# Performance work log

Measured on AMD Instinct MI355X. Metric: run time of the kernel, lower is better.

The kernel has to match this reference:

```python
import jax, jax.numpy as jnp
import numpy as np

N = 8192        # nodes in batch
E = 262144      # edges (avg degree 32)
IN_C = 64
OUT_C = 64
K = 3           # max_k
G = 64          # graphs in batch
NC = 10         # n_class
EPS = 1e-5      # batchnorm eps


def setup_inputs() -> dict:
    key = jax.random.key(0)
    ks = jax.random.split(key, 16)
    D_in = IN_C * K    # 192
    D_out = OUT_C * K  # 192
    inp = {
        'x': jax.random.normal(ks[0], (N, IN_C), jnp.float32),
        'edge_index': jax.random.randint(ks[1], (2, E), 0, N, dtype=jnp.int64),
        'batch': jnp.sort(jax.random.randint(ks[2], (N,), 0, G, dtype=jnp.int64)),
        # spectral-normed masked linear
        'W_orig': jax.random.normal(ks[3], (D_out, D_in), jnp.float32) * 0.05,
        'b': jnp.zeros((D_out,), jnp.float32),
        'u': jax.random.normal(ks[4], (D_out,), jnp.float32),
        # batchnorms (training-mode batch stats)
        'bn1_gamma': jnp.ones((D_out,), jnp.float32),
        'bn1_beta': jnp.zeros((D_out,), jnp.float32),
        'bn2_gamma': jnp.ones((D_out * 3,), jnp.float32),
        'bn2_beta': jnp.zeros((D_out * 3,), jnp.float32),
        # funnel head
        'w1': jax.random.normal(ks[5], (D_out * 2, D_out * 3), jnp.float32) * 0.05,
        'b1': jnp.zeros((D_out * 2,), jnp.float32),
        'w2': jax.random.normal(ks[6], (D_out, D_out * 2), jnp.float32) * 0.05,
        'b2': jnp.zeros((D_out,), jnp.float32),
        'w3': jax.random.normal(ks[7], (NC, D_out), jnp.float32) * 0.05,
        'b3': jnp.zeros((NC,), jnp.float32),
    }
    return inp


def _forward(x, edge_index, batch, W_orig, b, u, bn1_gamma, bn1_beta,
             bn2_gamma, bn2_beta, w1, b1, w2, b2, w3, b3):
    n = x.shape[0]
    row, col = edge_index[0], edge_index[1]
    # sym-normalized Laplacian L = I - D^-1/2 A D^-1/2, densified ([N,N])
    deg = jnp.zeros((n,), x.dtype).at[row].add(1.0)
    dinv = jnp.where(deg > 0, jax.lax.rsqrt(jnp.maximum(deg, 1.0)), 0.0)
    vals = -dinv[row] * dinv[col]
    L = jnp.zeros((n, n), x.dtype).at[row, col].add(vals)
    idx = jnp.arange(n)
    L = L.at[idx, idx].add(1.0)
    Hs = [x]
    h = x
    for _ in range(K - 1):
        h = L @ h
        Hs.append(h)
    Hcat = jnp.concatenate(Hs, axis=1)              # [N, IN_C*K]
    # spectral norm of W (one power-iteration step with stored u)
    v = W_orig.T @ u
    v = v / (jnp.linalg.norm(v) + 1e-12)
    sigma = u @ (W_orig @ v)
    W = W_orig / sigma
    # block lower-triangular mask: block i passes first IN_C*(i+1) input cols
    col_idx = jnp.arange(IN_C * K)
    row_block = jnp.arange(OUT_C * K) // OUT_C
    mask = (col_idx[None, :] < IN_C * (row_block[:, None] + 1)).astype(W.dtype)
    H = Hcat @ (W * mask).T + b                     # masked linear
    # reservoir_act_fun is identity (default)
    mu, var = H.mean(0), H.var(0)                   # BN (batch stats)
    H = bn1_gamma * (H - mu) * jax.lax.rsqrt(var + EPS) + bn1_beta
    # fused-style triple pooling over graph ids
    Hsum = jax.ops.segment_sum(H, batch, num_segments=G)
    cnt = jax.ops.segment_sum(jnp.ones((n,), H.dtype), batch, num_segments=G)
    Havg = Hsum / jnp.maximum(cnt, 1.0)[:, None]
    Hmax = jax.ops.segment_max(H, batch, num_segments=G)
    Hg = jnp.concatenate([Havg, Hsum, Hmax], axis=1)  # [G, 3*OUT_C*K]
    mu2, var2 = Hg.mean(0), Hg.var(0)
    xo = bn2_gamma * (Hg - mu2) * jax.lax.rsqrt(var2 + EPS) + bn2_beta
    # funnel output (dropout = identity in eval)
    xo = jax.nn.relu(xo @ w1.T + b1)
    xo = jax.nn.relu(xo @ w2.T + b2)
    return jax.nn.log_softmax(xo @ w3.T + b3, axis=1)


def reference(x, edge_index, batch, W_orig, b, u, bn1_gamma, bn1_beta,
              bn2_gamma, bn2_beta, w1, b1, w2, b2, w3, b3):
    return _forward(x, edge_index, batch, W_orig, b, u, bn1_gamma, bn1_beta,
                    bn2_gamma, bn2_beta, w1, b1, w2, b2, w3, b3)
```

## Files before the change

kernel.cpp:

```cpp
#include <hip/hip_runtime.h>
#include <math.h>

#define NN   8192
#define EE   262144
#define CIN  64
#define DD   192
#define GG   64
#define NCLS 10
#define D3   576
#define F1   384
#define F2   192
#define EPSB 1e-5f
#define NB   64
#define EPB  (EE / NB)
#define PS   8

__global__ __launch_bounds__(1024) void prep_kernel(const float* __restrict__ W,
    const float* __restrict__ u, const float* __restrict__ w1,
    const float* __restrict__ w2, const int* __restrict__ batch,
    const int* __restrict__ ei,
    float* __restrict__ sig, int* __restrict__ gstart, int* __restrict__ pcnt,
    float* __restrict__ Wp, float* __restrict__ Wp1, float* __restrict__ Wp2) {
    __shared__ int hist[NN];
    int b = blockIdx.x, t = threadIdx.x;
    if (b < 324) {
        int idx = b * 1024 + t;
        if (idx < DD * DD) {
            int r = idx / DD, c = idx - r * DD;
            float m = (c < CIN * ((r >> 6) + 1)) ? 1.f : 0.f;
            Wp[((c >> 2) * DD + r) * 4 + (c & 3)] = m * W[idx];
        } else if (idx < DD * DD + F1 * D3) {
            int i1 = idx - DD * DD;
            int tt = i1 / D3, k = i1 - tt * D3;
            Wp1[((k >> 2) * F1 + tt) * 4 + (k & 3)] = w1[i1];
        } else {
            int i2 = idx - DD * DD - F1 * D3;
            int tt = i2 / F1, k = i2 - tt * F1;
            Wp2[((k >> 2) * F2 + tt) * 4 + (k & 3)] = w2[i2];
        }
        return;
    }
    if (b == 325) {
        for (int i = t; i < NN; i += 1024) {
            int b0 = batch[i];
            int b1 = (i + 1 < NN) ? batch[i + 1] : GG;
            if (i == 0) { for (int g = 0; g <= b0; g++) gstart[g] = 0; }
            for (int g = b0 + 1; g <= b1; g++) gstart[g] = i + 1;
        }
        return;
    }
    if (b >= 326) {
        int cb = b - 326;
        int4* hz = (int4*)hist;
        for (int i = t; i < NN / 4; i += 1024) hz[i] = make_int4(0, 0, 0, 0);
        __syncthreads();
        int e0 = cb * EPB;
        for (int i = t; i < EPB; i += 1024) atomicAdd(&hist[ei[e0 + i]], 1);
        __syncthreads();
        const int4* hs = (const int4*)hist;
        int4* p4 = (int4*)&pcnt[cb * NN];
        for (int i = t; i < NN / 4; i += 1024) p4[i] = hs[i];
        return;
    }
    float* vp  = (float*)hist;
    float* vsh = vp + 768;
    float* red = vsh + DD;
    if (t < 768) {
        int c = t >> 2, j = t & 3;
        float s = 0.f;
        const float* Wc = W + c;
        for (int i = j * 48; i < j * 48 + 48; i++) s += Wc[i * DD] * u[i];
        vp[t] = s;
    }
    __syncthreads();
    float vv = 0.f;
    if (t < DD) {
        float v = vp[4 * t] + vp[4 * t + 1] + vp[4 * t + 2] + vp[4 * t + 3];
        vsh[t] = v;
        vv = v * v;
    }
    red[t] = vv;
    __syncthreads();
    for (int off = 512; off > 0; off >>= 1) {
        if (t < off) red[t] += red[t + off];
        __syncthreads();
    }
    float norm = sqrtf(red[0]) + 1e-12f;
    __syncthreads();
    float a = 0.f;
    for (int idx = t; idx < DD * DD; idx += 1024) {
        int r = idx / DD, c = idx - r * DD;
        a += u[r] * W[idx] * vsh[c];
    }
    red[t] = a;
    __syncthreads();
    for (int off = 512; off > 0; off >>= 1) {
        if (t < off) red[t] += red[t + off];
        __syncthreads();
    }
    if (t == 0) sig[0] = norm / red[0];
}

__global__ __launch_bounds__(256) void offs_kernel(int* __restrict__ pcnt,
                                                   int* __restrict__ deg,
                                                   float* __restrict__ dinv) {
    int i = blockIdx.x * 256 + threadIdx.x;
    int run = 0;
#pragma unroll
    for (int b = 0; b < NB; b++) {
        int v = pcnt[b * NN + i];
        pcnt[b * NN + i] = run;
        run += v;
    }
    deg[i] = run;
    dinv[i] = (run > 0) ? rsqrtf((float)run) : 0.f;
}

__global__ __launch_bounds__(1024) void scatter_kernel(const int* __restrict__ ei,
                                                       const int* __restrict__ deg,
                                                       const int* __restrict__ off,
                                                       int* __restrict__ rowptr,
                                                       unsigned short* __restrict__ csr_col) {
    __shared__ int cur[NN];
    __shared__ int temp[1024];
    int b = blockIdx.x, t = threadIdx.x;
    int base = t * 8;
    int d[8], l[8];
    {
        const int4 a4 = *(const int4*)&deg[base];
        const int4 b4 = *(const int4*)&deg[base + 4];
        d[0] = a4.x; d[1] = a4.y; d[2] = a4.z; d[3] = a4.w;
        d[4] = b4.x; d[5] = b4.y; d[6] = b4.z; d[7] = b4.w;
    }
    int run = 0;
#pragma unroll
    for (int j = 0; j < 8; j++) { l[j] = run; run += d[j]; }
    temp[t] = run;
    __syncthreads();
    for (int o = 1; o < 1024; o <<= 1) {
        int v = (t >= o) ? temp[t - o] : 0;
        __syncthreads();
        temp[t] += v;
        __syncthreads();
    }
    int prefix = (t > 0) ? temp[t - 1] : 0;
    const int* ob = &off[b * NN];
#pragma unroll
    for (int j = 0; j < 8; j++) cur[base + j] = prefix + l[j] + ob[base + j];
    if (b == 0) {
#pragma unroll
        for (int j = 0; j < 8; j++) rowptr[base + j] = prefix + l[j];
        if (t == 1023) rowptr[NN] = temp[1023];
    }
    __syncthreads();
    int e0 = b * EPB;
    for (int i = t; i < EPB; i += 1024) {
        int r = ei[e0 + i];
        int c = ei[EE + e0 + i];
        int pos = atomicAdd(&cur[r], 1);
        csr_col[pos] = (unsigned short)c;
    }
}

__global__ __launch_bounds__(256) void spmm_kernel(const float* __restrict__ hin,
    int in_stride, int in_off,
    const int* __restrict__ rowptr, const unsigned short* __restrict__ col,
    const float* __restrict__ dinv,
    float* __restrict__ Hcat, int coff, int write_self) {
    int idx = blockIdx.x * 256 + threadIdx.x;
    int row = idx >> 6;
    int lane = idx & 63;
    int s = rowptr[row], e = rowptr[row + 1];
    float acc0 = 0.f, acc1 = 0.f;
    int p = s;
    for (; p + 1 < e; p += 2) {
        int c0 = col[p], c1 = col[p + 1];
        acc0 += dinv[c0] * hin[c0 * in_stride + in_off + lane];
        acc1 += dinv[c1] * hin[c1 * in_stride + in_off + lane];
    }
    if (p < e) {
        int c = col[p];
        acc0 += dinv[c] * hin[c * in_stride + in_off + lane];
    }
    float acc = acc0 + acc1;
    float self = hin[row * in_stride + in_off + lane];
    Hcat[row * DD + coff + lane] = self - dinv[row] * acc;
    if (write_self) Hcat[row * DD + lane] = self;
}

__global__ __launch_bounds__(192) void gemm_kernel(float* __restrict__ Hcat,
    const float* __restrict__ Wp, const float* __restrict__ bias,
    const float* __restrict__ sig) {
    __shared__ float hs[16 * DD];
    int t = threadIdx.x;
    int n0 = blockIdx.x * 16;
    const float4* src = (const float4*)&Hcat[n0 * DD];
    float4* dst = (float4*)hs;
#pragma unroll
    for (int i = 0; i < 4; i++) dst[t + 192 * i] = src[t + 192 * i];
    __syncthreads();
    float acc[16];
#pragma unroll
    for (int r = 0; r < 16; r++) acc[r] = 0.f;
    const float4* Wp4 = (const float4*)Wp;
    for (int k4 = 0; k4 < DD / 4; k4++) {
        float4 w = Wp4[k4 * DD + t];
#pragma unroll
        for (int r = 0; r < 16; r++) {
            const float4 h = *(const float4*)&hs[r * DD + k4 * 4];
            acc[r] += h.x * w.x + h.y * w.y + h.z * w.z + h.w * w.w;
        }
    }
    float inv_sigma = sig[0];
    float bv = bias[t];
#pragma unroll
    for (int r = 0; r < 16; r++) Hcat[(n0 + r) * DD + t] = inv_sigma * acc[r] + bv;
}

__global__ __launch_bounds__(192) void pool_kernel(const float* __restrict__ H,
    const int* __restrict__ gstart,
    float* __restrict__ Psum, float* __restrict__ Psq,
    float* __restrict__ Pmin, float* __restrict__ Pmax) {
    int b = blockIdx.x;
    int g = b >> 3, s = b & 7, c = threadIdx.x;
    int beg = gstart[g], end = gstart[g + 1];
    float sum = 0.f, sq = 0.f, mn = INFINITY, mx = -INFINITY;
    for (int i = beg + s; i < end; i += PS) {
        float x = H[i * DD + c];
        sum += x; sq += x * x;
        mn = fminf(mn, x); mx = fmaxf(mx, x);
    }
    Psum[b * DD + c] = sum; Psq[b * DD + c] = sq;
    Pmin[b * DD + c] = mn;  Pmax[b * DD + c] = mx;
}

__global__ __launch_bounds__(64) void hg_kernel(
    const float* __restrict__ Psum, const float* __restrict__ Psq,
    const float* __restrict__ Pmin, const float* __restrict__ Pmax,
    const int* __restrict__ gstart,
    const float* __restrict__ g1, const float* __restrict__ be1,
    const float* __restrict__ g2, const float* __restrict__ be2,
    float* __restrict__ Hg) {
    int t = blockIdx.x;
    int g = threadIdx.x;
    int f = t / DD, c = t - f * DD;
    float Sg = 0.f, Qg = 0.f;
#pragma unroll
    for (int s = 0; s < PS; s++) {
        Sg += Psum[(g * PS + s) * DD + c];
        Qg += Psq[(g * PS + s) * DD + c];
    }
    float S = Sg, Q = Qg;
    for (int off = 32; off > 0; off >>= 1) {
        S += __shfl_xor(S, off);
        Q += __shfl_xor(Q, off);
    }
    float mu = S * (1.f / (float)NN);
    float var = Q * (1.f / (float)NN) - mu * mu;
    float sc = g1[c] * rsqrtf(var + EPSB);
    float bb = be1[c];
    float v;
    if (f == 2) {
        float mx = -INFINITY, mn = INFINITY;
#pragma unroll
        for (int s = 0; s < PS; s++) {
            mx = fmaxf(mx, Pmax[(g * PS + s) * DD + c]);
            mn = fminf(mn, Pmin[(g * PS + s) * DD + c]);
        }
        float raw = (sc >= 0.f) ? mx : mn;
        v = sc * (raw - mu) + bb;
    } else {
        float nf = (float)(gstart[g + 1] - gstart[g]);
        float hsum = sc * (Sg - nf * mu) + nf * bb;
        v = (f == 0) ? hsum / fmaxf(nf, 1.f) : hsum;
    }
    float s2 = v, ss2 = v * v;
    for (int off = 32; off > 0; off >>= 1) {
        s2 += __shfl_xor(s2, off);
        ss2 += __shfl_xor(ss2, off);
    }
    float m2 = s2 * (1.f / (float)GG);
    float var2 = ss2 * (1.f / (float)GG) - m2 * m2;
    float sc2 = g2[t] * rsqrtf(var2 + EPSB);
    Hg[g * D3 + t] = sc2 * (v - m2) + be2[t];
}

__global__ __launch_bounds__(F1) void funnel_kernel(const float* __restrict__ Hg,
    const float* __restrict__ Wp1, const float* __restrict__ b1,
    const float* __restrict__ Wp2, const float* __restrict__ b2,
    const float* __restrict__ w3, const float* __restrict__ b3,
    float* __restrict__ out) {
    __shared__ float hg[D3];
    __shared__ float x1[F1];
    __shared__ float x2[F2];
    __shared__ float lg[NCLS];
    __shared__ float s_lse;
    int g = blockIdx.x, t = threadIdx.x;
    for (int i = t; i < D3; i += F1) hg[i] = Hg[g * D3 + i];
    __syncthreads();
    {
        float a = b1[t];
        const float4* W4 = (const float4*)Wp1;
        for (int k4 = 0; k4 < D3 / 4; k4++) {
            float4 w = W4[k4 * F1 + t];
            const float4 h = *(const float4*)&hg[k4 * 4];
            a += w.x * h.x + w.y * h.y + w.z * h.z + w.w * h.w;
        }
        x1[t] = fmaxf(a, 0.f);
    }
    __syncthreads();
    if (t < F2) {
        float a = b2[t];
        const float4* W4 = (const float4*)Wp2;
        for (int k4 = 0; k4 < F1 / 4; k4++) {
            float4 w = W4[k4 * F2 + t];
            const float4 h = *(const float4*)&x1[k4 * 4];
            a += w.x * h.x + w.y * h.y + w.z * h.z + w.w * h.w;
        }
        x2[t] = fmaxf(a, 0.f);
    }
    __syncthreads();
    if (t < NCLS) {
        float a = b3[t];
        const float4* wr = (const float4*)&w3[t * F2];
        const float4* h4 = (const float4*)x2;
        for (int k = 0; k < F2 / 4; k++) {
            float4 w = wr[k], h = h4[k];
            a += w.x * h.x + w.y * h.y + w.z * h.z + w.w * h.w;
        }
        lg[t] = a;
    }
    __syncthreads();
    if (t == 0) {
        float m = lg[0];
        for (int i = 1; i < NCLS; i++) m = fmaxf(m, lg[i]);
        float se = 0.f;
        for (int i = 0; i < NCLS; i++) se += expf(lg[i] - m);
        s_lse = m + logf(se);
    }
    __syncthreads();
    if (t < NCLS) out[g * NCLS + t] = lg[t] - s_lse;
}


extern "C" void kernel_launch(void* const* d_in, const int* in_sizes, int n_in,
                              void* d_out, int out_size, void* d_ws, size_t ws_size,
                              hipStream_t stream) {
    (void)in_sizes; (void)n_in; (void)out_size; (void)ws_size;
    const float* x     = (const float*)d_in[0];
    const int*   ei    = (const int*)d_in[1];
    const int*   batch = (const int*)d_in[2];
    const float* W     = (const float*)d_in[3];
    const float* b     = (const float*)d_in[4];
    const float* u     = (const float*)d_in[5];
    const float* g1    = (const float*)d_in[6];
    const float* be1   = (const float*)d_in[7];
    const float* g2    = (const float*)d_in[8];
    const float* be2   = (const float*)d_in[9];
    const float* w1    = (const float*)d_in[10];
    const float* b1    = (const float*)d_in[11];
    const float* w2    = (const float*)d_in[12];
    const float* b2    = (const float*)d_in[13];
    const float* w3    = (const float*)d_in[14];
    const float* b3    = (const float*)d_in[15];
    float* out = (float*)d_out;
    char*  ws  = (char*)d_ws;

    int*            gstart  = (int*)(ws + 0);
    int*            rowptr  = (int*)(ws + 512);
    int*            deg     = (int*)(ws + 33536);
    float*          dinv    = (float*)(ws + 66304);
    float*          sig     = (float*)(ws + 99072);
    float*          Wp      = (float*)(ws + 99328);
    float*          Psum    = (float*)(ws + 246784);
    float*          Psq     = (float*)(ws + 640000);
    float*          Pmin    = (float*)(ws + 1033216);
    float*          Pmax    = (float*)(ws + 1426432);
    float*          Hg      = (float*)(ws + 1819648);
    unsigned short* csr_col = (unsigned short*)(ws + 1967104);
    float*          Wp1     = (float*)(ws + 2491392);
    float*          Wp2     = (float*)(ws + 3376128);
    int*            pcnt    = (int*)(ws + 3671040);
    float*          Hcat    = (float*)(ws + 5768192);

    prep_kernel<<<326 + NB, 1024, 0, stream>>>(W, u, w1, w2, batch, ei,
                                               sig, gstart, pcnt, Wp, Wp1, Wp2);
    offs_kernel<<<NN / 256, 256, 0, stream>>>(pcnt, deg, dinv);
    scatter_kernel<<<NB, 1024, 0, stream>>>(ei, deg, pcnt, rowptr, csr_col);
    spmm_kernel<<<NN * 64 / 256, 256, 0, stream>>>(x, CIN, 0, rowptr, csr_col, dinv, Hcat, CIN, 1);
    spmm_kernel<<<NN * 64 / 256, 256, 0, stream>>>(Hcat, DD, CIN, rowptr, csr_col, dinv, Hcat, 2 * CIN, 0);
    gemm_kernel<<<NN / 16, 192, 0, stream>>>(Hcat, Wp, b, sig);
    pool_kernel<<<GG * PS, 192, 0, stream>>>(Hcat, gstart, Psum, Psq, Pmin, Pmax);
    hg_kernel<<<D3, 64, 0, stream>>>(Psum, Psq, Pmin, Pmax, gstart, g1, be1, g2, be2, Hg);
    funnel_kernel<<<GG, F1, 0, stream>>>(Hg, Wp1, b1, Wp2, b2, w3, b3, out);
}
```

Baseline: 200.3 us.

## Fuse masked GEMM with graph pooling via atomics; shrink partial counts to u16

The GEMM and pooling kernels are merged. Each GEMM block reduces its rows per graph and updates global per-graph sum, sum-of-squares, and max/min through atomics, using order-preserving uint keys for float max/min. The final H is no longer written back to Hcat, and the separate pooling pass is gone. Per-block edge histograms are stored as uint16 to halve that traffic, and the SpMM loop unrolls to four edges. The changes add global atomic contention and a zero-init pass in prep, and they make the floating-point summation order nondeterministic.

```diff
diff --git a/kernel.cpp b/kernel.cpp
--- a/kernel.cpp
+++ b/kernel.cpp
@@ -13,14 +13,24 @@
 #define EPSB 1e-5f
 #define NB   64
 #define EPB  (EE / NB)
-#define PS   8
+
+__device__ __forceinline__ unsigned int fkey(float f) {
+    unsigned int b = __float_as_uint(f);
+    return b ^ (0x80000000u | (unsigned int)((int)b >> 31));
+}
+__device__ __forceinline__ float fdec(unsigned int k) {
+    unsigned int b = k ^ ((k & 0x80000000u) ? 0x80000000u : 0xFFFFFFFFu);
+    return __uint_as_float(b);
+}
 
 __global__ __launch_bounds__(1024) void prep_kernel(const float* __restrict__ W,
     const float* __restrict__ u, const float* __restrict__ w1,
     const float* __restrict__ w2, const int* __restrict__ batch,
     const int* __restrict__ ei,
-    float* __restrict__ sig, int* __restrict__ gstart, int* __restrict__ pcnt,
-    float* __restrict__ Wp, float* __restrict__ Wp1, float* __restrict__ Wp2) {
+    float* __restrict__ sig, int* __restrict__ gstart,
+    unsigned short* __restrict__ pcnt,
+    float* __restrict__ Wp, float* __restrict__ Wp1, float* __restrict__ Wp2,
+    int* __restrict__ pinit) {
     __shared__ int hist[NN];
     int b = blockIdx.x, t = threadIdx.x;
     if (b < 324) {
@@ -49,6 +59,13 @@
         }
         return;
     }
+    if (b == 326 + NB) {
+        int4* z = (int4*)pinit;
+        for (int i = t; i < 3 * GG * DD / 4; i += 1024) z[i] = make_int4(0, 0, 0, 0);
+        int4* m = (int4*)(pinit + 3 * GG * DD);
+        for (int i = t; i < GG * DD / 4; i += 1024) m[i] = make_int4(-1, -1, -1, -1);
+        return;
+    }
     if (b >= 326) {
         int cb = b - 326;
         int4* hz = (int4*)hist;
@@ -57,9 +74,12 @@
         int e0 = cb * EPB;
         for (int i = t; i < EPB; i += 1024) atomicAdd(&hist[ei[e0 + i]], 1);
         __syncthreads();
-        const int4* hs = (const int4*)hist;
-        int4* p4 = (int4*)&pcnt[cb * NN];
-        for (int i = t; i < NN / 4; i += 1024) p4[i] = hs[i];
+        const int2* h2 = (const int2*)hist;
+        ushort2* q2 = (ushort2*)&pcnt[cb * NN];
+        for (int i = t; i < NN / 2; i += 1024) {
+            int2 h = h2[i];
+            q2[i] = make_ushort2((unsigned short)h.x, (unsigned short)h.y);
+        }
         return;
     }
     float* vp  = (float*)hist;
@@ -101,7 +121,7 @@
     if (t == 0) sig[0] = norm / red[0];
 }
 
-__global__ __launch_bounds__(256) void offs_kernel(int* __restrict__ pcnt,
+__global__ __launch_bounds__(256) void offs_kernel(unsigned short* __restrict__ pcnt,
                                                    int* __restrict__ deg,
                                                    float* __restrict__ dinv) {
     int i = blockIdx.x * 256 + threadIdx.x;
@@ -109,7 +129,7 @@
 #pragma unroll
     for (int b = 0; b < NB; b++) {
         int v = pcnt[b * NN + i];
-        pcnt[b * NN + i] = run;
+        pcnt[b * NN + i] = (unsigned short)run;
         run += v;
     }
     deg[i] = run;
@@ -118,7 +138,7 @@
 
 __global__ __launch_bounds__(1024) void scatter_kernel(const int* __restrict__ ei,
                                                        const int* __restrict__ deg,
-                                                       const int* __restrict__ off,
+                                                       const unsigned short* __restrict__ off,
                                                        int* __restrict__ rowptr,
                                                        unsigned short* __restrict__ csr_col) {
     __shared__ int cur[NN];
@@ -144,9 +164,18 @@
         __syncthreads();
     }
     int prefix = (t > 0) ? temp[t - 1] : 0;
-    const int* ob = &off[b * NN];
-#pragma unroll
-    for (int j = 0; j < 8; j++) cur[base + j] = prefix + l[j] + ob[base + j];
+    {
+        const unsigned short* ob = &off[b * NN];
+        int4 opk = *(const int4*)(ob + base);
+        cur[base + 0] = prefix + l[0] + (opk.x & 0xFFFF);
+        cur[base + 1] = prefix + l[1] + (int)((unsigned)opk.x >> 16);
+        cur[base + 2] = prefix + l[2] + (opk.y & 0xFFFF);
+        cur[base + 3] = prefix + l[3] + (int)((unsigned)opk.y >> 16);
+        cur[base + 4] = prefix + l[4] + (opk.z & 0xFFFF);
+        cur[base + 5] = prefix + l[5] + (int)((unsigned)opk.z >> 16);
+        cur[base + 6] = prefix + l[6] + (opk.w & 0xFFFF);
+        cur[base + 7] = prefix + l[7] + (int)((unsigned)opk.w >> 16);
+    }
     if (b == 0) {
 #pragma unroll
         for (int j = 0; j < 8; j++) rowptr[base + j] = prefix + l[j];
@@ -171,72 +200,83 @@
     int row = idx >> 6;
     int lane = idx & 63;
     int s = rowptr[row], e = rowptr[row + 1];
-    float acc0 = 0.f, acc1 = 0.f;
+    float acc0 = 0.f, acc1 = 0.f, acc2 = 0.f, acc3 = 0.f;
     int p = s;
-    for (; p + 1 < e; p += 2) {
-        int c0 = col[p], c1 = col[p + 1];
+    for (; p + 3 < e; p += 4) {
+        int c0 = col[p], c1 = col[p + 1], c2 = col[p + 2], c3 = col[p + 3];
         acc0 += dinv[c0] * hin[c0 * in_stride + in_off + lane];
         acc1 += dinv[c1] * hin[c1 * in_stride + in_off + lane];
-    }
-    if (p < e) {
+        acc2 += dinv[c2] * hin[c2 * in_stride + in_off + lane];
+        acc3 += dinv[c3] * hin[c3 * in_stride + in_off + lane];
+    }
+    for (; p < e; p++) {
         int c = col[p];
         acc0 += dinv[c] * hin[c * in_stride + in_off + lane];
     }
-    float acc = acc0 + acc1;
+    float acc = (acc0 + acc1) + (acc2 + acc3);
     float self = hin[row * in_stride + in_off + lane];
     Hcat[row * DD + coff + lane] = self - dinv[row] * acc;
     if (write_self) Hcat[row * DD + lane] = self;
 }
 
-__global__ __launch_bounds__(192) void gemm_kernel(float* __restrict__ Hcat,
+__global__ __launch_bounds__(384) void gemm_pool_kernel(const float* __restrict__ Hcat,
     const float* __restrict__ Wp, const float* __restrict__ bias,
-    const float* __restrict__ sig) {
+    const float* __restrict__ sig, const int* __restrict__ batch,
+    float* __restrict__ Psum, float* __restrict__ Psq,
+    unsigned int* __restrict__ Pmaxk, unsigned int* __restrict__ Pmink) {
     __shared__ float hs[16 * DD];
+    __shared__ int bb[16];
     int t = threadIdx.x;
     int n0 = blockIdx.x * 16;
     const float4* src = (const float4*)&Hcat[n0 * DD];
     float4* dst = (float4*)hs;
-#pragma unroll
-    for (int i = 0; i < 4; i++) dst[t + 192 * i] = src[t + 192 * i];
-    __syncthreads();
-    float acc[16];
-#pragma unroll
-    for (int r = 0; r < 16; r++) acc[r] = 0.f;
+    dst[t] = src[t];
+    dst[t + 384] = src[t + 384];
+    if (t < 16) bb[t] = batch[n0 + t];
+    __syncthreads();
+    int half = t / 192;
+    int ch = t - half * 192;
+    int r0 = half * 8;
+    float acc[8];
+#pragma unroll
+    for (int r = 0; r < 8; r++) acc[r] = 0.f;
     const float4* Wp4 = (const float4*)Wp;
+    const float* hb = &hs[r0 * DD];
     for (int k4 = 0; k4 < DD / 4; k4++) {
-        float4 w = Wp4[k4 * DD + t];
-#pragma unroll
-        for (int r = 0; r < 16; r++) {
-            const float4 h = *(const float4*)&hs[r * DD + k4 * 4];
+        float4 w = Wp4[k4 * DD + ch];
+#pragma unroll
+        for (int r = 0; r < 8; r++) {
+            const float4 h = *(const float4*)&hb[r * DD + k4 * 4];
             acc[r] += h.x * w.x + h.y * w.y + h.z * w.z + h.w * w.w;
         }
     }
     float inv_sigma = sig[0];
-    float bv = bias[t];
-#pragma unroll
-    for (int r = 0; r < 16; r++) Hcat[(n0 + r) * DD + t] = inv_sigma * acc[r] + bv;
-}
-
-__global__ __launch_bounds__(192) void pool_kernel(const float* __restrict__ H,
-    const int* __restrict__ gstart,
-    float* __restrict__ Psum, float* __restrict__ Psq,
-    float* __restrict__ Pmin, float* __restrict__ Pmax) {
-    int b = blockIdx.x;
-    int g = b >> 3, s = b & 7, c = threadIdx.x;
-    int beg = gstart[g], end = gstart[g + 1];
+    float bv = bias[ch];
+    int gcur = bb[r0];
     float sum = 0.f, sq = 0.f, mn = INFINITY, mx = -INFINITY;
-    for (int i = beg + s; i < end; i += PS) {
-        float x = H[i * DD + c];
-        sum += x; sq += x * x;
-        mn = fminf(mn, x); mx = fmaxf(mx, x);
-    }
-    Psum[b * DD + c] = sum; Psq[b * DD + c] = sq;
-    Pmin[b * DD + c] = mn;  Pmax[b * DD + c] = mx;
+#pragma unroll
+    for (int r = 0; r < 8; r++) {
+        float v = inv_sigma * acc[r] + bv;
+        int g = bb[r0 + r];
+        if (g != gcur) {
+            atomicAdd(&Psum[gcur * DD + ch], sum);
+            atomicAdd(&Psq[gcur * DD + ch], sq);
+            atomicMax(&Pmaxk[gcur * DD + ch], fkey(mx));
+            atomicMin(&Pmink[gcur * DD + ch], fkey(mn));
+            sum = 0.f; sq = 0.f; mn = INFINITY; mx = -INFINITY; gcur = g;
+        }
+        sum += v; sq += v * v;
+        mn = fminf(mn, v); mx = fmaxf(mx, v);
+    }
+    atomicAdd(&Psum[gcur * DD + ch], sum);
+    atomicAdd(&Psq[gcur * DD + ch], sq);
+    atomicMax(&Pmaxk[gcur * DD + ch], fkey(mx));
+    atomicMin(&Pmink[gcur * DD + ch], fkey(mn));
 }
 
 __global__ __launch_bounds__(64) void hg_kernel(
     const float* __restrict__ Psum, const float* __restrict__ Psq,
-    const float* __restrict__ Pmin, const float* __restrict__ Pmax,
+    const unsigned int* __restrict__ Pmaxk, const unsigned int* __restrict__ Pmink,
     const int* __restrict__ gstart,
     const float* __restrict__ g1, const float* __restrict__ be1,
     const float* __restrict__ g2, const float* __restrict__ be2,
@@ -244,12 +284,8 @@
     int t = blockIdx.x;
     int g = threadIdx.x;
     int f = t / DD, c = t - f * DD;
-    float Sg = 0.f, Qg = 0.f;
-#pragma unroll
-    for (int s = 0; s < PS; s++) {
-        Sg += Psum[(g * PS + s) * DD + c];
-        Qg += Psq[(g * PS + s) * DD + c];
-    }
+    float Sg = Psum[g * DD + c];
+    float Qg = Psq[g * DD + c];
     float S = Sg, Q = Qg;
     for (int off = 32; off > 0; off >>= 1) {
         S += __shfl_xor(S, off);
@@ -261,12 +297,8 @@
     float bb = be1[c];
     float v;
     if (f == 2) {
-        float mx = -INFINITY, mn = INFINITY;
-#pragma unroll
-        for (int s = 0; s < PS; s++) {
-            mx = fmaxf(mx, Pmax[(g * PS + s) * DD + c]);
-            mn = fminf(mn, Pmin[(g * PS + s) * DD + c]);
-        }
+        float mx = fdec(Pmaxk[g * DD + c]);
+        float mn = fdec(Pmink[g * DD + c]);
         float raw = (sc >= 0.f) ? mx : mn;
         v = sc * (raw - mu) + bb;
     } else {
@@ -373,24 +405,25 @@
     float*          sig     = (float*)(ws + 99072);
     float*          Wp      = (float*)(ws + 99328);
     float*          Psum    = (float*)(ws + 246784);
-    float*          Psq     = (float*)(ws + 640000);
-    float*          Pmin    = (float*)(ws + 1033216);
-    float*          Pmax    = (float*)(ws + 1426432);
-    float*          Hg      = (float*)(ws + 1819648);
-    unsigned short* csr_col = (unsigned short*)(ws + 1967104);
-    float*          Wp1     = (float*)(ws + 2491392);
-    float*          Wp2     = (float*)(ws + 3376128);
-    int*            pcnt    = (int*)(ws + 3671040);
-    float*          Hcat    = (float*)(ws + 5768192);
-
-    prep_kernel<<<326 + NB, 1024, 0, stream>>>(W, u, w1, w2, batch, ei,
-                                               sig, gstart, pcnt, Wp, Wp1, Wp2);
+    float*          Psq     = (float*)(ws + 295936);
+    unsigned int*   Pmaxk   = (unsigned int*)(ws + 345088);
+    unsigned int*   Pmink   = (unsigned int*)(ws + 394240);
+    float*          Hg      = (float*)(ws + 443392);
+    unsigned short* csr_col = (unsigned short*)(ws + 590848);
+    float*          Wp1     = (float*)(ws + 1115136);
+    float*          Wp2     = (float*)(ws + 1999872);
+    unsigned short* pcnt    = (unsigned short*)(ws + 2294784);
+    float*          Hcat    = (float*)(ws + 3343360);
+
+    prep_kernel<<<326 + NB + 1, 1024, 0, stream>>>(W, u, w1, w2, batch, ei,
+                                                   sig, gstart, pcnt, Wp, Wp1, Wp2,
+                                                   (int*)Psum);
     offs_kernel<<<NN / 256, 256, 0, stream>>>(pcnt, deg, dinv);
     scatter_kernel<<<NB, 1024, 0, stream>>>(ei, deg, pcnt, rowptr, csr_col);
     spmm_kernel<<<NN * 64 / 256, 256, 0, stream>>>(x, CIN, 0, rowptr, csr_col, dinv, Hcat, CIN, 1);
     spmm_kernel<<<NN * 64 / 256, 256, 0, stream>>>(Hcat, DD, CIN, rowptr, csr_col, dinv, Hcat, 2 * CIN, 0);
-    gemm_kernel<<<NN / 16, 192, 0, stream>>>(Hcat, Wp, b, sig);
-    pool_kernel<<<GG * PS, 192, 0, stream>>>(Hcat, gstart, Psum, Psq, Pmin, Pmax);
-    hg_kernel<<<D3, 64, 0, stream>>>(Psum, Psq, Pmin, Pmax, gstart, g1, be1, g2, be2, Hg);
+    gemm_pool_kernel<<<NN / 16, 384, 0, stream>>>(Hcat, Wp, b, sig, batch,
+                                                  Psum, Psq, Pmaxk, Pmink);
+    hg_kernel<<<D3, 64, 0, stream>>>(Psum, Psq, Pmaxk, Pmink, gstart, g1, be1, g2, be2, Hg);
     funnel_kernel<<<GG, F1, 0, stream>>>(Hg, Wp1, b1, Wp2, b2, w3, b3, out);
 }
```

Measured after the change: 181.7 us. -9.3%, faster.
